# Kernel optimization log

Hardware: AMD Instinct MI355X
Metric: run time of the kernel (lower is better)

Reference implementation:

```python
import jax, jax.numpy as jnp
import numpy as np

NNODES = 8192
K = 512
NEG_SLOPE = 0.01  # torch F.leaky_relu default
EPS = 1e-12       # torch F.normalize default eps


def setup_inputs() -> dict:
    key = jax.random.key(0)
    kx, kp = jax.random.split(key)
    x = jax.random.normal(kx, (NNODES, K), dtype=jnp.float32)
    # xavier_uniform init for proto (nnodes, k)
    bound = float(np.sqrt(6.0 / (NNODES + K)))
    proto = jax.random.uniform(kp, (NNODES, K), dtype=jnp.float32,
                               minval=-bound, maxval=bound)
    return {"x": x, "proto": proto}


def reference(x, proto):
    # In-place no_grad step in torch: proto <- l2norm(proto), rows unit-norm.
    norm = jnp.sqrt(jnp.sum(proto * proto, axis=1, keepdims=True))
    pn = proto / jnp.maximum(norm, EPS)  # (nnodes, k), unit rows
    # cosine_similarity over all pairs == pn @ pn.T since rows are unit-norm.
    # This fuses torch's (nnodes, nnodes, k) broadcast into one GEMM.
    sim = jnp.einsum('ik,jk->ij', pn, pn)  # (nnodes, nnodes)
    return jnp.where(sim >= 0, sim, NEG_SLOPE * sim)
```

## Files before the change

### kernel.cpp

```cpp
#include <hip/hip_runtime.h>
#include <stdint.h>

#define NN 8192
#define KD 512
#define BM 128
#define BK 32
#define NTILE (NN / BM)
#define NTRI (NTILE * (NTILE + 1) / 2)
#define NKT (KD / BK)

typedef __bf16 bf16;
typedef __bf16 bf16x8 __attribute__((ext_vector_type(8)));
typedef float f32x4 __attribute__((ext_vector_type(4)));

__global__ __launch_bounds__(256) void rownorm_kernel(const float* __restrict__ proto,
                                                      bf16* __restrict__ pn) {
    const int row  = blockIdx.x * 4 + (threadIdx.x >> 6);
    const int lane = threadIdx.x & 63;
    const float4* src = (const float4*)(proto + (size_t)row * KD) + lane * 2;
    const float4 v0 = src[0];
    const float4 v1 = src[1];
    float s = v0.x*v0.x + v0.y*v0.y + v0.z*v0.z + v0.w*v0.w
            + v1.x*v1.x + v1.y*v1.y + v1.z*v1.z + v1.w*v1.w;
#pragma unroll
    for (int off = 32; off; off >>= 1) s += __shfl_xor(s, off);
    const float inv = 1.0f / fmaxf(sqrtf(s), 1e-12f);
    bf16x8 o;
    o[0] = (bf16)(v0.x*inv); o[1] = (bf16)(v0.y*inv);
    o[2] = (bf16)(v0.z*inv); o[3] = (bf16)(v0.w*inv);
    o[4] = (bf16)(v1.x*inv); o[5] = (bf16)(v1.y*inv);
    o[6] = (bf16)(v1.z*inv); o[7] = (bf16)(v1.w*inv);
    *(bf16x8*)(pn + (size_t)row * KD + lane * 8) = o;
}

__device__ __forceinline__ void gload_lds16(const bf16* g, bf16* l) {
    __builtin_amdgcn_global_load_lds(
        (const __attribute__((address_space(1))) void*)g,
        (__attribute__((address_space(3))) void*)l, 16, 0, 0);
}

__device__ __forceinline__ float lrelu(float v) {
    return (v >= 0.0f) ? v : 0.01f * v;
}

__global__ __launch_bounds__(256, 4) void gemm_sym_kernel(const bf16* __restrict__ P,
                                                          float* __restrict__ C) {
    __shared__ bf16 sA[2][BM * BK];
    __shared__ bf16 sB[2][BM * BK];

    const int bid = blockIdx.x;
    const int swz = (bid & 7) * (NTRI / 8) + (bid >> 3);
    int tm = 0, rem = swz;
    while (rem >= NTILE - tm) { rem -= NTILE - tm; ++tm; }
    const int tn = tm + rem;

    const int tid  = threadIdx.x;
    const int w    = tid >> 6;
    const int lane = tid & 63;
    const int rowA0 = tm * BM;
    const int rowB0 = tn * BM;
    const int wm = (w >> 1) * 64;
    const int wn = (w & 1) * 64;
    const int rr = lane & 15;
    const int h  = lane >> 4;

    const int swcol = ((tid & 3) ^ ((tid >> 3) & 3)) * 8;
    const bf16* gA = P + (size_t)(rowA0 + (tid >> 2)) * KD + swcol;
    const bf16* gB = P + (size_t)(rowB0 + (tid >> 2)) * KD + swcol;
    const int stL = w * 512;

    const int swf  = (h ^ ((rr >> 1) & 3)) * 8;
    const int aOff = (wm + rr) * 32 + swf;
    const int bOff = (wn + rr) * 32 + swf;

    f32x4 acc[4][4] = {};

#define STAGE(buf, kt)                                              \
    do {                                                            \
        gload_lds16(gA + (kt),           &sA[buf][0] + stL);        \
        gload_lds16(gA + 64 * KD + (kt), &sA[buf][0] + stL + 2048); \
        gload_lds16(gB + (kt),           &sB[buf][0] + stL);        \
        gload_lds16(gB + 64 * KD + (kt), &sB[buf][0] + stL + 2048); \
    } while (0)

#define COMPUTE(buf)                                                        \
    do {                                                                    \
        bf16x8 af[4], bfr[4];                                               \
        _Pragma("unroll")                                                   \
        for (int m = 0; m < 4; ++m)                                         \
            af[m] = *(const bf16x8*)(&sA[buf][0] + aOff + m * 512);         \
        _Pragma("unroll")                                                   \
        for (int n = 0; n < 4; ++n)                                         \
            bfr[n] = *(const bf16x8*)(&sB[buf][0] + bOff + n * 512);        \
        _Pragma("unroll")                                                   \
        for (int m = 0; m < 4; ++m)                                         \
            _Pragma("unroll")                                               \
            for (int n = 0; n < 4; ++n)                                     \
                acc[m][n] = __builtin_amdgcn_mfma_f32_16x16x32_bf16(        \
                    af[m], bfr[n], acc[m][n], 0, 0, 0);                     \
    } while (0)

    STAGE(0, 0);
    __syncthreads();

#pragma unroll
    for (int t = 0; t < NKT; ++t) {
        if (t < NKT - 1) STAGE((t + 1) & 1, (t + 1) * BK);
        COMPUTE(t & 1);
        if (t < NKT - 1) __syncthreads();
    }

    const int cr = h * 4;
    const int cc = rr;

#pragma unroll
    for (int m = 0; m < 4; ++m)
#pragma unroll
        for (int n = 0; n < 4; ++n)
#pragma unroll
            for (int r = 0; r < 4; ++r)
                C[(size_t)(rowA0 + wm + m * 16 + cr + r) * NN
                  + (rowB0 + wn + n * 16 + cc)] = lrelu(acc[m][n][r]);

    if (tm != tn) {
#pragma unroll
        for (int m = 0; m < 4; ++m)
#pragma unroll
            for (int n = 0; n < 4; ++n) {
                float4 vv;
                vv.x = lrelu(acc[m][n][0]);
                vv.y = lrelu(acc[m][n][1]);
                vv.z = lrelu(acc[m][n][2]);
                vv.w = lrelu(acc[m][n][3]);
                *(float4*)&C[(size_t)(rowB0 + wn + n * 16 + cc) * NN
                             + (rowA0 + wm + m * 16 + cr)] = vv;
            }
    }
#undef STAGE
#undef COMPUTE
}

extern "C" void kernel_launch(void* const* d_in, const int* in_sizes, int n_in,
                              void* d_out, int out_size, void* d_ws, size_t ws_size,
                              hipStream_t stream) {
    const float* proto = (const float*)d_in[1];
    float* C  = (float*)d_out;
    bf16* pn  = (bf16*)d_ws;

    rownorm_kernel<<<dim3(NN / 4), dim3(256), 0, stream>>>(proto, pn);
    gemm_sym_kernel<<<dim3(NTRI), dim3(256), 0, stream>>>(pn, C);
}
```

Baseline: 102.9 us.

## Enlarge symmetric GEMM tiles to 256x256 with BK 64 and 8 waves

Doubles the output tile edge to 256 and the K-step to 64, and moves to 512-thread blocks with 8 waves in a 2x4 grid, each holding an 8x4 set of MFMA accumulators. The LDS swizzle and the fragment loads are reworked for the 64-wide K slice, and each slice is split into two 32-K MFMA halves. The goal is more operand reuse per global and LDS load, and less redundant work on diagonal tiles. The cost is a much larger LDS footprint (about 128KB per block), which likely limits residency to one block per CU. The grid also shrinks to 528 blocks, which can leave an uneven tail across CUs.

```diff
diff --git a/kernel.cpp b/kernel.cpp
--- a/kernel.cpp
+++ b/kernel.cpp
@@ -3,8 +3,8 @@
 
 #define NN 8192
 #define KD 512
-#define BM 128
-#define BK 32
+#define BM 256
+#define BK 64
 #define NTILE (NN / BM)
 #define NTRI (NTILE * (NTILE + 1) / 2)
 #define NKT (KD / BK)
@@ -43,7 +43,7 @@
     return (v >= 0.0f) ? v : 0.01f * v;
 }
 
-__global__ __launch_bounds__(256, 4) void gemm_sym_kernel(const bf16* __restrict__ P,
+__global__ __launch_bounds__(512, 2) void gemm_sym_kernel(const bf16* __restrict__ P,
                                                           float* __restrict__ C) {
     __shared__ bf16 sA[2][BM * BK];
     __shared__ bf16 sB[2][BM * BK];
@@ -57,47 +57,65 @@
     const int tid  = threadIdx.x;
     const int w    = tid >> 6;
     const int lane = tid & 63;
+    const int wr = w >> 2;
+    const int wc = w & 3;
     const int rowA0 = tm * BM;
     const int rowB0 = tn * BM;
-    const int wm = (w >> 1) * 64;
-    const int wn = (w & 1) * 64;
     const int rr = lane & 15;
     const int h  = lane >> 4;
+    const int sw = rr & 7;
 
-    const int swcol = ((tid & 3) ^ ((tid >> 3) & 3)) * 8;
-    const bf16* gA = P + (size_t)(rowA0 + (tid >> 2)) * KD + swcol;
-    const bf16* gB = P + (size_t)(rowB0 + (tid >> 2)) * KD + swcol;
+    const int swcol = ((tid & 7) ^ ((tid >> 3) & 7)) * 8;
+    const bf16* gA = P + (size_t)(rowA0 + (tid >> 3)) * KD + swcol;
+    const bf16* gB = P + (size_t)(rowB0 + (tid >> 3)) * KD + swcol;
     const int stL = w * 512;
 
-    const int swf  = (h ^ ((rr >> 1) & 3)) * 8;
-    const int aOff = (wm + rr) * 32 + swf;
-    const int bOff = (wn + rr) * 32 + swf;
+    const int cA0 = ((h ^ sw) << 3);
+    const int aBase = (wr * 128 + rr) * 64 + cA0;
+    const int bBase = (wc * 64 + rr) * 64 + cA0;
 
-    f32x4 acc[4][4] = {};
+    f32x4 acc[8][4] = {};
 
-#define STAGE(buf, kt)                                              \
-    do {                                                            \
-        gload_lds16(gA + (kt),           &sA[buf][0] + stL);        \
-        gload_lds16(gA + 64 * KD + (kt), &sA[buf][0] + stL + 2048); \
-        gload_lds16(gB + (kt),           &sB[buf][0] + stL);        \
-        gload_lds16(gB + 64 * KD + (kt), &sB[buf][0] + stL + 2048); \
+#define STAGE(buf, kt)                                                     \
+    do {                                                                   \
+        _Pragma("unroll")                                                  \
+        for (int l = 0; l < 4; ++l) {                                      \
+            gload_lds16(gA + (size_t)l * 64 * KD + (kt),                   \
+                        &sA[buf][0] + l * 4096 + stL);                     \
+            gload_lds16(gB + (size_t)l * 64 * KD + (kt),                   \
+                        &sB[buf][0] + l * 4096 + stL);                     \
+        }                                                                  \
     } while (0)
 
 #define COMPUTE(buf)                                                        \
     do {                                                                    \
-        bf16x8 af[4], bfr[4];                                               \
+        const bf16* ra_ = &sA[buf][0];                                      \
+        const bf16* rb_ = &sB[buf][0];                                      \
+        bf16x8 bf_[4][2];                                                   \
         _Pragma("unroll")                                                   \
-        for (int m = 0; m < 4; ++m)                                         \
-            af[m] = *(const bf16x8*)(&sA[buf][0] + aOff + m * 512);         \
+        for (int n = 0; n < 4; ++n) {                                       \
+            bf_[n][0] = *(const bf16x8*)(rb_ + bBase + n * 1024);           \
+            bf_[n][1] = *(const bf16x8*)(rb_ + ((bBase + n * 1024) ^ 32));  \
+        }                                                                   \
         _Pragma("unroll")                                                   \
-        for (int n = 0; n < 4; ++n)                                         \
-            bfr[n] = *(const bf16x8*)(&sB[buf][0] + bOff + n * 512);        \
-        _Pragma("unroll")                                                   \
-        for (int m = 0; m < 4; ++m)                                         \
+        for (int mq = 0; mq < 4; ++mq) {                                    \
+            bf16x8 af_[2][2];                                               \
             _Pragma("unroll")                                               \
-            for (int n = 0; n < 4; ++n)                                     \
-                acc[m][n] = __builtin_amdgcn_mfma_f32_16x16x32_bf16(        \
-                    af[m], bfr[n], acc[m][n], 0, 0, 0);                     \
+            for (int mi = 0; mi < 2; ++mi) {                                \
+                const int ro = aBase + (mq * 2 + mi) * 1024;                \
+                af_[mi][0] = *(const bf16x8*)(ra_ + ro);                    \
+                af_[mi][1] = *(const bf16x8*)(ra_ + (ro ^ 32));             \
+            }                                                               \
+            _Pragma("unroll")                                               \
+            for (int mi = 0; mi < 2; ++mi)                                  \
+                _Pragma("unroll")                                           \
+                for (int n = 0; n < 4; ++n) {                               \
+                    acc[mq*2+mi][n] = __builtin_amdgcn_mfma_f32_16x16x32_bf16( \
+                        af_[mi][0], bf_[n][0], acc[mq*2+mi][n], 0, 0, 0);   \
+                    acc[mq*2+mi][n] = __builtin_amdgcn_mfma_f32_16x16x32_bf16( \
+                        af_[mi][1], bf_[n][1], acc[mq*2+mi][n], 0, 0, 0);   \
+                }                                                           \
+        }                                                                   \
     } while (0)
 
     STAGE(0, 0);
@@ -114,17 +132,17 @@
     const int cc = rr;
 
 #pragma unroll
-    for (int m = 0; m < 4; ++m)
+    for (int m = 0; m < 8; ++m)
 #pragma unroll
         for (int n = 0; n < 4; ++n)
 #pragma unroll
             for (int r = 0; r < 4; ++r)
-                C[(size_t)(rowA0 + wm + m * 16 + cr + r) * NN
-                  + (rowB0 + wn + n * 16 + cc)] = lrelu(acc[m][n][r]);
+                C[(size_t)(rowA0 + wr * 128 + m * 16 + cr + r) * NN
+                  + (rowB0 + wc * 64 + n * 16 + cc)] = lrelu(acc[m][n][r]);
 
     if (tm != tn) {
 #pragma unroll
-        for (int m = 0; m < 4; ++m)
+        for (int m = 0; m < 8; ++m)
 #pragma unroll
             for (int n = 0; n < 4; ++n) {
                 float4 vv;
@@ -132,8 +150,8 @@
                 vv.y = lrelu(acc[m][n][1]);
                 vv.z = lrelu(acc[m][n][2]);
                 vv.w = lrelu(acc[m][n][3]);
-                *(float4*)&C[(size_t)(rowB0 + wn + n * 16 + cc) * NN
-                             + (rowA0 + wm + m * 16 + cr)] = vv;
+                *(float4*)&C[(size_t)(rowB0 + wc * 64 + n * 16 + cc) * NN
+                             + (rowA0 + wr * 128 + m * 16 + cr)] = vv;
             }
     }
 #undef STAGE
@@ -148,5 +166,5 @@
     bf16* pn  = (bf16*)d_ws;
 
     rownorm_kernel<<<dim3(NN / 4), dim3(256), 0, stream>>>(proto, pn);
-    gemm_sym_kernel<<<dim3(NTRI), dim3(256), 0, stream>>>(pn, C);
+    gemm_sym_kernel<<<dim3(NTRI), dim3(512), 0, stream>>>(pn, C);
 }
```

Result: slower. 114.7 us (+11.5%).

## Enlarge symmetric GEMM tiles to 256 with a 4-stage LDS pipeline

Applied to the files above, without the earlier changes.

Doubles the block tile to 256x256 with 512 threads and 8 waves. It replaces the double buffer with a 4-deep global_load_lds prefetch ring synchronised by explicit vmcnt waits and raw barriers, and raises wave priority around the MFMA bursts. The goal is more operand reuse per tile and more latency hiding. In exchange the LDS XOR swizzle is dropped, which risks bank conflicts. The ring uses about 128KB of LDS, which limits occupancy to one block per CU. Output stores, likely the dominant cost, are unchanged.

```diff
diff --git a/kernel.cpp b/kernel.cpp
--- a/kernel.cpp
+++ b/kernel.cpp
@@ -3,7 +3,7 @@
 
 #define NN 8192
 #define KD 512
-#define BM 128
+#define BM 256
 #define BK 32
 #define NTILE (NN / BM)
 #define NTRI (NTILE * (NTILE + 1) / 2)
@@ -43,10 +43,9 @@
     return (v >= 0.0f) ? v : 0.01f * v;
 }
 
-__global__ __launch_bounds__(256, 4) void gemm_sym_kernel(const bf16* __restrict__ P,
+__global__ __launch_bounds__(512, 2) void gemm_sym_kernel(const bf16* __restrict__ P,
                                                           float* __restrict__ C) {
-    __shared__ bf16 sA[2][BM * BK];
-    __shared__ bf16 sB[2][BM * BK];
+    __shared__ bf16 sm[4][2][BM * BK];
 
     const int bid = blockIdx.x;
     const int swz = (bid & 7) * (NTRI / 8) + (bid >> 3);
@@ -57,74 +56,87 @@
     const int tid  = threadIdx.x;
     const int w    = tid >> 6;
     const int lane = tid & 63;
+    const int wr = w >> 2;
+    const int wc = w & 3;
     const int rowA0 = tm * BM;
     const int rowB0 = tn * BM;
-    const int wm = (w >> 1) * 64;
-    const int wn = (w & 1) * 64;
     const int rr = lane & 15;
     const int h  = lane >> 4;
 
-    const int swcol = ((tid & 3) ^ ((tid >> 3) & 3)) * 8;
-    const bf16* gA = P + (size_t)(rowA0 + (tid >> 2)) * KD + swcol;
-    const bf16* gB = P + (size_t)(rowB0 + (tid >> 2)) * KD + swcol;
+    const bf16* gA = P + (size_t)(rowA0 + (tid >> 2)) * KD + (tid & 3) * 8;
+    const bf16* gB = P + (size_t)(rowB0 + (tid >> 2)) * KD + (tid & 3) * 8;
     const int stL = w * 512;
 
-    const int swf  = (h ^ ((rr >> 1) & 3)) * 8;
-    const int aOff = (wm + rr) * 32 + swf;
-    const int bOff = (wn + rr) * 32 + swf;
+    const int aBase = (wr * 128 + rr) * BK + h * 8;
+    const int bBase = (wc * 64  + rr) * BK + h * 8;
 
-    f32x4 acc[4][4] = {};
+    f32x4 acc[8][4] = {};
 
-#define STAGE(buf, kt)                                              \
-    do {                                                            \
-        gload_lds16(gA + (kt),           &sA[buf][0] + stL);        \
-        gload_lds16(gA + 64 * KD + (kt), &sA[buf][0] + stL + 2048); \
-        gload_lds16(gB + (kt),           &sB[buf][0] + stL);        \
-        gload_lds16(gB + 64 * KD + (kt), &sB[buf][0] + stL + 2048); \
+#define VMCNT(n) asm volatile("s_waitcnt vmcnt(" #n ")" ::: "memory")
+
+#define STAGE(s_)                                                       \
+    do {                                                                \
+        bf16* a_ = &sm[(s_) & 3][0][0];                                 \
+        bf16* b_ = &sm[(s_) & 3][1][0];                                 \
+        const int kt_ = (s_) * BK;                                      \
+        gload_lds16(gA + kt_,            a_ + stL);                     \
+        gload_lds16(gA + 128 * KD + kt_, a_ + stL + 4096);              \
+        gload_lds16(gB + kt_,            b_ + stL);                     \
+        gload_lds16(gB + 128 * KD + kt_, b_ + stL + 4096);              \
     } while (0)
 
-#define COMPUTE(buf)                                                        \
+#define COMPUTE(s_)                                                         \
     do {                                                                    \
-        bf16x8 af[4], bfr[4];                                               \
+        const bf16* ra_ = &sm[(s_) & 3][0][0];                              \
+        const bf16* rb_ = &sm[(s_) & 3][1][0];                              \
+        bf16x8 af[8], bfr[4];                                               \
         _Pragma("unroll")                                                   \
-        for (int m = 0; m < 4; ++m)                                         \
-            af[m] = *(const bf16x8*)(&sA[buf][0] + aOff + m * 512);         \
+        for (int m = 0; m < 8; ++m)                                         \
+            af[m] = *(const bf16x8*)(ra_ + aBase + m * 512);                \
         _Pragma("unroll")                                                   \
         for (int n = 0; n < 4; ++n)                                         \
-            bfr[n] = *(const bf16x8*)(&sB[buf][0] + bOff + n * 512);        \
+            bfr[n] = *(const bf16x8*)(rb_ + bBase + n * 512);               \
+        __builtin_amdgcn_s_setprio(1);                                      \
         _Pragma("unroll")                                                   \
-        for (int m = 0; m < 4; ++m)                                         \
+        for (int m = 0; m < 8; ++m)                                         \
             _Pragma("unroll")                                               \
             for (int n = 0; n < 4; ++n)                                     \
                 acc[m][n] = __builtin_amdgcn_mfma_f32_16x16x32_bf16(        \
                     af[m], bfr[n], acc[m][n], 0, 0, 0);                     \
+        __builtin_amdgcn_s_setprio(0);                                      \
     } while (0)
 
-    STAGE(0, 0);
-    __syncthreads();
+    STAGE(0); STAGE(1); STAGE(2);
 
 #pragma unroll
-    for (int t = 0; t < NKT; ++t) {
-        if (t < NKT - 1) STAGE((t + 1) & 1, (t + 1) * BK);
-        COMPUTE(t & 1);
-        if (t < NKT - 1) __syncthreads();
+    for (int s = 0; s < NKT; ++s) {
+        if (s + 3 < NKT) STAGE(s + 3);
+        if (s <= NKT - 3) VMCNT(8);
+        else if (s == NKT - 2) VMCNT(4);
+        else VMCNT(0);
+        __builtin_amdgcn_s_barrier();
+        COMPUTE(s);
+        if (s < NKT - 1) __builtin_amdgcn_s_barrier();
     }
+#undef STAGE
+#undef COMPUTE
+#undef VMCNT
 
     const int cr = h * 4;
     const int cc = rr;
 
 #pragma unroll
-    for (int m = 0; m < 4; ++m)
+    for (int m = 0; m < 8; ++m)
 #pragma unroll
         for (int n = 0; n < 4; ++n)
 #pragma unroll
             for (int r = 0; r < 4; ++r)
-                C[(size_t)(rowA0 + wm + m * 16 + cr + r) * NN
-                  + (rowB0 + wn + n * 16 + cc)] = lrelu(acc[m][n][r]);
+                C[(size_t)(rowA0 + wr * 128 + m * 16 + cr + r) * NN
+                  + (rowB0 + wc * 64 + n * 16 + cc)] = lrelu(acc[m][n][r]);
 
     if (tm != tn) {
 #pragma unroll
-        for (int m = 0; m < 4; ++m)
+        for (int m = 0; m < 8; ++m)
 #pragma unroll
             for (int n = 0; n < 4; ++n) {
                 float4 vv;
@@ -132,12 +144,10 @@
                 vv.y = lrelu(acc[m][n][1]);
                 vv.z = lrelu(acc[m][n][2]);
                 vv.w = lrelu(acc[m][n][3]);
-                *(float4*)&C[(size_t)(rowB0 + wn + n * 16 + cc) * NN
-                             + (rowA0 + wm + m * 16 + cr)] = vv;
+                *(float4*)&C[(size_t)(rowB0 + wc * 64 + n * 16 + cc) * NN
+                             + (rowA0 + wr * 128 + m * 16 + cr)] = vv;
             }
     }
-#undef STAGE
-#undef COMPUTE
 }
 
 extern "C" void kernel_launch(void* const* d_in, const int* in_sizes, int n_in,
@@ -148,5 +158,5 @@
     bf16* pn  = (bf16*)d_ws;
 
     rownorm_kernel<<<dim3(NN / 4), dim3(256), 0, stream>>>(proto, pn);
-    gemm_sym_kernel<<<dim3(NTRI), dim3(256), 0, stream>>>(pn, C);
+    gemm_sym_kernel<<<dim3(NTRI), dim3(512), 0, stream>>>(pn, C);
 }
```

Result: slower. 109.6 us (+6.5%).
